# Kernel optimization log

Hardware: AMD Instinct MI355X
Metric: run time of the kernel (lower is better)

## Reference

```python
import jax, jax.numpy as jnp
import numpy as np

N = 65536          # query points (rays * samples per chunk)
C = 2048           # num_codes in code cloud
K = 16             # knn neighbors
CD = 64            # code_dim
IN_XYZ = 63        # positional-encoded xyz channels
IN_DIR = 27        # positional-encoded dir channels
W = 128            # decoder width (D=4, skips=[2])
DIST_SCALE = 2.0


def setup_inputs() -> dict:
    key = jax.random.key(0)
    ks = jax.random.split(key, 16)

    def glorot(k, shape):
        return jax.random.normal(k, shape, jnp.float32) / np.float32(np.sqrt(shape[0]))

    in_x = CD + IN_XYZ  # decoder in_channels_xyz = 127
    inp = {
        "indices": jnp.zeros((1,), jnp.int32),
        "query_points": jax.random.uniform(ks[0], (N, 3), jnp.float32),
        "xyzdir_embedded": jax.random.normal(ks[1], (N, IN_XYZ + IN_DIR), jnp.float32),
        "codes_position": jax.random.uniform(ks[2], (1, C, 3), jnp.float32),
        "codes": jax.random.normal(ks[3], (1, C, CD), jnp.float32) * 0.01,
        # decoder params
        "W0": glorot(ks[4], (in_x, W)), "b0": jnp.zeros((W,), jnp.float32),
        "W1": glorot(ks[5], (W, W)), "b1": jnp.zeros((W,), jnp.float32),
        "W2": glorot(ks[6], (W + in_x, W)), "b2": jnp.zeros((W,), jnp.float32),  # skip layer i=2
        "W3": glorot(ks[7], (W, W)), "b3": jnp.zeros((W,), jnp.float32),
        "Wf": glorot(ks[8], (W, W)), "bf": jnp.zeros((W,), jnp.float32),          # xyz_encoding_final
        "Wd": glorot(ks[9], (W + IN_DIR, W // 2)), "bd": jnp.zeros((W // 2,), jnp.float32),
        "Ws": glorot(ks[10], (W, 1)), "bs": jnp.zeros((1,), jnp.float32),
        "Wr": glorot(ks[11], (W // 2, 3)), "br": jnp.zeros((3,), jnp.float32),
    }
    return inp


def _knn_idx(q, c, k):
    # brute-force L2 knn (faiss replacement); indices only, no grad (torch no_grad)
    q = jax.lax.stop_gradient(q)
    c = jax.lax.stop_gradient(c)
    d2 = (jnp.sum(q * q, -1, keepdims=True)
          - 2.0 * q @ c.T
          + jnp.sum(c * c, -1))  # (N, C)
    _, idx = jax.lax.top_k(-d2, k)  # (N, K) nearest
    return idx


def reference(indices, query_points, xyzdir_embedded, codes_position, codes,
              W0, b0, W1, b1, W2, b2, W3, b3, Wf, bf, Wd, bd, Ws, bs, Wr, br):
    # --- CodeCloud.query ---
    cp = codes_position[indices][0]      # (C, 3)
    cc = codes[indices][0]               # (C, CD)
    idx = _knn_idx(query_points, cp, K)  # (N, K)
    neigh_pos = cp[idx]                  # (N, K, 3)
    sq = jnp.sum((query_points[:, None, :] - neigh_pos) ** 2, -1) + 1e-16  # (N, K)
    w = 1.0 / jnp.sqrt(sq) ** DIST_SCALE
    w = w / jnp.sum(w, -1, keepdims=True)
    neigh_codes = cc[idx]                # (N, K, CD)
    query_codes = jnp.einsum("nk,nkd->nd", w, neigh_codes)  # (N, CD)

    # --- IM_Decoder (D=4, W=128, skips=[2]) ---
    x = jnp.concatenate([query_codes, xyzdir_embedded], -1)  # (N, 127+27)
    in_x = CD + IN_XYZ
    input_xyz, input_dir = x[:, :in_x], x[:, in_x:]
    h = jax.nn.relu(input_xyz @ W0 + b0)
    h = jax.nn.relu(h @ W1 + b1)
    h = jax.nn.relu(jnp.concatenate([input_xyz, h], -1) @ W2 + b2)  # skip at i=2
    h = jax.nn.relu(h @ W3 + b3)
    sigma = h @ Ws + bs                       # (N, 1)
    final = h @ Wf + bf                       # (N, W)
    d = jax.nn.relu(jnp.concatenate([final, input_dir], -1) @ Wd + bd)
    rgb = d @ Wr + br                         # (N, 3)
    return jnp.concatenate([rgb, sigma], -1)  # (N, 4)
```

## Files before the change

kernel.cpp:

```cpp
#include <hip/hip_runtime.h>

#define N_Q   65536
#define N_C   2048
#define KNN_K 16
#define CDIM  64
#define SLCAP 128
#define KINF  0x7FFFFFFF
#define WSZ   108544

#define GN     16
#define GCELLS 4096
#define LCAP   448
#define LSTORE 512
#define NSLOT  8

typedef _Float16 half_t;
typedef float v4f __attribute__((ext_vector_type(4)));
typedef half_t v8h __attribute__((ext_vector_type(8)));
typedef unsigned short u16x8 __attribute__((ext_vector_type(8)));

#define ASTRIDE 136
#define DSTRIDE 40

__device__ __forceinline__ int dppx(int v, int j){
  if (j == 1) return __builtin_amdgcn_mov_dpp(v, 0xB1,  0xF, 0xF, true);
  if (j == 2) return __builtin_amdgcn_mov_dpp(v, 0x4E,  0xF, 0xF, true);
  if (j == 8) return __builtin_amdgcn_mov_dpp(v, 0x128, 0xF, 0xF, true);
  return __shfl_xor(v, j, 64);
}
__device__ __forceinline__ float dppxf(float v, int j){
  return __int_as_float(dppx(__float_as_int(v), j));
}

__device__ __forceinline__ int select16th(int x){
  int P = 0;
#pragma unroll
  for (int b = 30; b >= 0; --b){
    int cand = P | (1 << b);
    unsigned long long m = __ballot(x < cand);
    if ((int)__popcll(m) < 16) P = cand;
  }
  return P;
}

__device__ __forceinline__ int select16_tau(int x){
  int P = 0;
#pragma unroll
  for (int b = 30; b >= 11; --b){
    int cand = P | (1 << b);
    unsigned long long m = __ballot(x < cand);
    if ((int)__popcll(m) < 16) P = cand;
  }
  return P | 0x7FF;
}

__device__ __forceinline__ int knn_fallback(const float4* lp, float nqx,
                                            float nqy, float nqz, int lane){
  unsigned used = 0u;
  int keep = KINF;
#pragma unroll 1
  for (int rr = 0; rr < KNN_K; rr++){
    int best = KINF;
#pragma unroll 1
    for (int j = 0; j < 32; j++){
      int c = j*64 + lane;
      float4 P = lp[c];
      float s = fmaf(P.x, nqx, fmaf(P.y, nqy, fmaf(P.z, nqz, P.w)));
      int pv = (__float_as_int(s) & 0xFFFFF800) | c;
      pv = ((used >> j) & 1u) ? KINF : pv;
      best = min(best, pv);
    }
    int gm = best;
#pragma unroll
    for (int off2 = 1; off2 < 64; off2 <<= 1)
      gm = min(gm, __shfl_xor(gm, off2, 64));
    if (lane == rr) keep = gm;
    int gc = gm & 0x7FF;
    if ((gc & 63) == lane) used |= (1u << (gc >> 6));
  }
  return keep;
}

__global__ void wtrans_kernel(const float* W0, const float* W1, const float* W2,
                              const float* W3, const float* Wf, const float* Wd,
                              const int* indices, const float* cpos,
                              half_t* wt, float4* cpos4){
  int idx = blockIdx.x * 256 + threadIdx.x;
  if (idx >= 110592) return;
  if (idx >= WSZ){
    int i = idx - WSZ;
    const float* cp = cpos + (size_t)indices[0] * N_C * 3;
    float x = cp[i*3 + 0], y = cp[i*3 + 1], z = cp[i*3 + 2];
    cpos4[i] = make_float4(x, y, z, fmaf(x, x, fmaf(y, y, fmaf(z, z, 4.0f))));
    return;
  }
  int base, nt, mode;
  const float* src = W1;
  if (idx < 16384){ base = 0; nt = 8; mode = 1; }
  else if (idx < 32768){ base = 16384; nt = 8; mode = 0; src = W1; }
  else if (idx < 65536){ base = 32768; nt = 8; mode = 2; }
  else if (idx < 81920){ base = 65536; nt = 8; mode = 0; src = W3; }
  else if (idx < 98304){ base = 81920; nt = 8; mode = 0; src = Wf; }
  else { base = 98304; nt = 4; mode = 3; }
  int i = idx - base;
  int tile = i >> 9, e = i & 511;
  int lane = e >> 3, j = e & 7;
  int k0idx = tile / nt, tcol = tile - k0idx*nt;
  int n = tcol*16 + (lane & 15);
  int k = k0idx*32 + ((lane >> 4) << 3) + j;
  float val;
  if (mode == 0)      val = src[k*128 + n];
  else if (mode == 1) val = (k < 127) ? W0[k*128 + n] : 0.f;
  else if (mode == 2) val = (k == 127) ? 0.f
                           : ((k < 127) ? W2[k*128 + n] : W2[(k-1)*128 + n]);
  else                val = (k < 155) ? Wd[k*64 + n] : 0.f;
  wt[idx] = (half_t)val;
}

__global__ __launch_bounds__(512) void grid_kernel(const float4* cpos4,
    unsigned short* list, int* cnt){
  int lane = threadIdx.x & 63, wave = threadIdx.x >> 6;
  int c = blockIdx.x * 8 + wave;
  int cx = c & 15, cy = (c >> 4) & 15, cz = c >> 8;
  int lox = min(max(cx - 4, 0), 7);
  int loy = min(max(cy - 4, 0), 7);
  int loz = min(max(cz - 4, 0), 7);
  unsigned short* L = list + (size_t)c * LSTORE;
  int n = 0;
#pragma unroll 1
  for (int b = 0; b < 32; b++){
    int i = b * 64 + lane;
    float4 P = cpos4[i];
    int ix = min((int)(P.x * 16.0f), 15);
    int iy = min((int)(P.y * 16.0f), 15);
    int iz = min((int)(P.z * 16.0f), 15);
    bool in = ((unsigned)(ix - lox) < 9u) && ((unsigned)(iy - loy) < 9u) &&
              ((unsigned)(iz - loz) < 9u);
    unsigned long long m = __ballot(in);
    if (m){
      int mb = __builtin_amdgcn_mbcnt_hi((unsigned)(m >> 32),
               __builtin_amdgcn_mbcnt_lo((unsigned)m, 0));
      if (in && (n + mb) < LCAP) L[n + mb] = (unsigned short)i;
      n += (int)__popcll(m);
    }
  }
  if (lane == 0) cnt[c] = (n <= LCAP) ? n : 0;
}

__global__ __launch_bounds__(512, 6) void knn_kernel(const int* indices,
    const float* qpts, const float4* cpos4, const unsigned short* list,
    const int* cnt, const float* codes, const float* xyzdir,
    half_t* Ain, half_t* Din){
  __shared__ float4 lp[N_C];
  __shared__ int    sl[8*SLCAP];
  int tid = threadIdx.x;
  int lane = tid & 63, wave = tid >> 6;
  const float* cc = codes + (size_t)indices[0] * N_C * CDIM;

  for (int c = tid; c < N_C; c += 512) lp[c] = cpos4[c];
  __syncthreads();

  int q = blockIdx.x * 8 + wave;
  float qx = qpts[q*3 + 0];
  float qy = qpts[q*3 + 1];
  float qz = qpts[q*3 + 2];
  float nqx = -2.0f*qx, nqy = -2.0f*qy, nqz = -2.0f*qz;
  float qq = fmaf(qx, qx, fmaf(qy, qy, qz*qz));

  int cx = min((int)(qx * 16.0f), 15);
  int cy = min((int)(qy * 16.0f), 15);
  int cz = min((int)(qz * 16.0f), 15);
  int cell = cx | (cy << 4) | (cz << 8);
  int lox = min(max(cx - 4, 0), 7);
  int loy = min(max(cy - 4, 0), 7);
  int loz = min(max(cz - 4, 0), 7);
  int nl = cnt[cell];

  u16x8 cand8 = *(const u16x8*)(list + (size_t)cell * LSTORE + lane * 8);

  int p[NSLOT];
  int lanemin = KINF;
#pragma unroll
  for (int s = 0; s < NSLOT; s++){
    int j = lane*8 + s;
    int idx = (int)cand8[s] & 2047;
    float4 P = lp[idx];
    float sc = fmaf(P.x, nqx, fmaf(P.y, nqy, fmaf(P.z, nqz, P.w)));
    int pv = (__float_as_int(sc) & 0xFFFFF800) | idx;
    pv = (j < nl) ? pv : KINF;
    asm("" : "+v"(pv));
    p[s] = pv;
    lanemin = min(lanemin, pv);
  }

  int tau = select16_tau(lanemin);

  int* slw = &sl[wave * SLCAP];
  int n = 0;
#pragma unroll
  for (int s = 0; s < NSLOT; s++){
    bool c = (p[s] <= tau);
    unsigned long long m = __ballot(c);
    if (m){
      if (n <= 64){
        if (c){
          int mb = __builtin_amdgcn_mbcnt_hi((unsigned)(m >> 32),
                   __builtin_amdgcn_mbcnt_lo((unsigned)m, 0));
          slw[n + mb] = p[s];
        }
      }
      n += (int)__popcll(m);
    }
  }
  __builtin_amdgcn_wave_barrier();

  int keep = KINF;
  bool need_fb = true;
  if (n >= KNN_K && n <= 64){
    int x = (lane < n) ? slw[lane] : KINF;
    int P2 = select16th(x);
    unsigned long long wmask = __ballot(x <= P2);
    int pos = __builtin_amdgcn_mbcnt_hi((unsigned)(wmask >> 32),
              __builtin_amdgcn_mbcnt_lo((unsigned)wmask, 0));
    if (x <= P2) slw[pos] = x;
    __builtin_amdgcn_wave_barrier();
    keep = (lane < KNN_K) ? slw[lane] : KINF;

    float d2u = __int_as_float(P2 & 0xFFFFF800) - 4.0f + qq + 0.002f;
    float lofx = lox * 0.0625f, lofy = loy * 0.0625f, lofz = loz * 0.0625f;
    float cl = 1e9f;
    if (lox > 0) cl = fminf(cl, qx - lofx);
    if (lox < 7) cl = fminf(cl, lofx + 0.5625f - qx);
    if (loy > 0) cl = fminf(cl, qy - lofy);
    if (loy < 7) cl = fminf(cl, lofy + 0.5625f - qy);
    if (loz > 0) cl = fminf(cl, qz - lofz);
    if (loz < 7) cl = fminf(cl, lofz + 0.5625f - qz);
    need_fb = !(d2u <= cl * cl);
  }
  if (need_fb) keep = knn_fallback(lp, nqx, nqy, nqz, lane);

  int ci = keep & 0x7FF;
  float4 P = lp[ci];
  float dx = qx - P.x, dy = qy - P.y, dz = qz - P.z;
  float d2 = fmaf(dz, dz, fmaf(dy, dy, dx*dx));
  float w = 1.0f / (d2 + 1e-16f);
  float wm = (lane < KNN_K) ? w : 0.0f;
  wm += dppxf(wm, 1);
  wm += dppxf(wm, 2);
  wm += __shfl_xor(wm, 4, 64);
  wm += dppxf(wm, 8);
  float wn = w / wm;

  if (lane < KNN_K){
    slw[64 + 2*lane]     = ci;
    slw[64 + 2*lane + 1] = __float_as_int(wn);
  }
  __builtin_amdgcn_wave_barrier();

  float acc = 0.f;
#pragma unroll
  for (int i = 0; i < KNN_K; i++){
    int   cb = slw[64 + 2*i];
    float wb = __int_as_float(slw[64 + 2*i + 1]);
    acc = fmaf(wb, cc[cb*CDIM + lane], acc);
  }
  size_t arow = (size_t)q * ASTRIDE;
  Ain[arow + lane] = (half_t)acc;

  float xv = (lane < 63) ? xyzdir[(size_t)q*90 + lane] : 0.f;
  Ain[arow + 64 + lane] = (half_t)xv;
  if (lane < 8) Ain[arow + 128 + lane] = (half_t)0.f;
  if (lane < 40){
    float dv = (lane < 27) ? xyzdir[(size_t)q*90 + 63 + lane] : 0.f;
    Din[(size_t)q*DSTRIDE + lane] = (half_t)dv;
  }
}

template<int NCH, int NT>
__device__ inline void mfma_pl(const half_t* act, int astride, int rowbase,
                               const half_t* wlayer, int nt, int ktbase,
                               int tcolbase, v4f acc[2][NT], int lane){
  v8h breg[NCH*NT];
#pragma unroll
  for (int c = 0; c < NCH; c++){
#pragma unroll
    for (int t = 0; t < NT; t++){
      const half_t* bp = wlayer +
          ((size_t)(((ktbase + c)*nt + tcolbase + t) << 9) + (lane << 3));
      breg[c*NT + t] = *(const v8h*)bp;
    }
  }
  int m = lane & 15, quad = lane >> 4;
#pragma unroll
  for (int c = 0; c < NCH; c++){
    v8h a0 = *(const v8h*)&act[(rowbase + m)*astride + c*32 + quad*8];
    v8h a1 = *(const v8h*)&act[(rowbase + 16 + m)*astride + c*32 + quad*8];
#pragma unroll
    for (int t = 0; t < NT; t++){
      acc[0][t] = __builtin_amdgcn_mfma_f32_16x16x32_f16(a0, breg[c*NT + t], acc[0][t], 0, 0, 0);
      acc[1][t] = __builtin_amdgcn_mfma_f32_16x16x32_f16(a1, breg[c*NT + t], acc[1][t], 0, 0, 0);
    }
  }
}

template<int NT>
__device__ inline void epilogue64(v4f acc[2][NT], half_t* outb, int rowbase,
                                  int colbase, const float* bias, bool relu,
                                  int lane){
  int n = lane & 15, quad = lane >> 4;
#pragma unroll
  for (int t = 0; t < NT; t++){
    int col = colbase + t*16 + n;
    float bv = bias[col];
#pragma unroll
    for (int g = 0; g < 2; g++){
#pragma unroll
      for (int r = 0; r < 4; r++){
        float v = acc[g][t][r] + bv;
        if (relu) v = fmaxf(v, 0.f);
        outb[(rowbase + g*16 + quad*4 + r)*ASTRIDE + col] = (half_t)v;
      }
    }
  }
}

__global__ __launch_bounds__(512, 6) void mlp_mfma(
    const half_t* Ain, const half_t* Din, const half_t* wt,
    const float* b0, const float* b1, const float* b2, const float* b3,
    const float* bfb, const float* bdb,
    const float* Wsb, const float* bsb, const float* Wrb, const float* brb,
    float* out){
  __shared__ __align__(16) half_t Abuf[64*ASTRIDE];
  __shared__ __align__(16) half_t Pbuf[64*ASTRIDE];
  __shared__ __align__(16) half_t Qbuf[64*ASTRIDE];

  int tid = threadIdx.x, lane = tid & 63, wave = tid >> 6;
  int qbase = blockIdx.x * 64;

  for (int i = tid; i < 64*17; i += 512){
    int r = i / 17, c8 = i - r*17;
    *(uint4*)&Abuf[r*ASTRIDE + (c8 << 3)] =
        *(const uint4*)&Ain[(size_t)(qbase + r)*ASTRIDE + (c8 << 3)];
  }
  __syncthreads();

  int rowbase  = (wave >> 2) * 32;
  int colq     = wave & 3;
  int colbase  = colq * 32;
  int tcolbase = colq * 2;
  v4f acc[2][2];
  v4f accd[2][1];

  const half_t* wt0 = wt;
  const half_t* wt1 = wt + 16384;
  const half_t* wt2 = wt + 32768;
  const half_t* wt3 = wt + 65536;
  const half_t* wtf = wt + 81920;
  const half_t* wtd = wt + 98304;

#define ZACC22() { for (int g_ = 0; g_ < 2; g_++) for (int t_ = 0; t_ < 2; t_++) \
                   for (int e_ = 0; e_ < 4; e_++) acc[g_][t_][e_] = 0.f; }

  ZACC22();
  mfma_pl<4,2>(Abuf, ASTRIDE, rowbase, wt0, 8, 0, tcolbase, acc, lane);
  epilogue64<2>(acc, Pbuf, rowbase, colbase, b0, true, lane);
  __syncthreads();

  ZACC22();
  mfma_pl<4,2>(Pbuf, ASTRIDE, rowbase, wt1, 8, 0, tcolbase, acc, lane);
  epilogue64<2>(acc, Qbuf, rowbase, colbase, b1, true, lane);
  __syncthreads();

  ZACC22();
  mfma_pl<4,2>(Abuf, ASTRIDE, rowbase, wt2, 8, 0, tcolbase, acc, lane);
  mfma_pl<4,2>(Qbuf, ASTRIDE, rowbase, wt2, 8, 4, tcolbase, acc, lane);
  epilogue64<2>(acc, Pbuf, rowbase, colbase, b2, true, lane);
  __syncthreads();

  ZACC22();
  mfma_pl<4,2>(Pbuf, ASTRIDE, rowbase, wt3, 8, 0, tcolbase, acc, lane);
  epilogue64<2>(acc, Abuf, rowbase, colbase, b3, true, lane);
  __syncthreads();

  ZACC22();
  mfma_pl<4,2>(Abuf, ASTRIDE, rowbase, wtf, 8, 0, tcolbase, acc, lane);
  epilogue64<2>(acc, Pbuf, rowbase, colbase, bfb, false, lane);
  __syncthreads();

#pragma unroll
  for (int g_ = 0; g_ < 2; g_++)
#pragma unroll
    for (int e_ = 0; e_ < 4; e_++) accd[g_][0][e_] = 0.f;
  mfma_pl<4,1>(Pbuf, ASTRIDE, rowbase, wtd, 4, 0, colq, accd, lane);
  mfma_pl<1,1>(Din + (size_t)qbase*DSTRIDE, DSTRIDE, rowbase, wtd, 4, 4, colq,
               accd, lane);
  epilogue64<1>(accd, Qbuf, rowbase, colq * 16, bdb, true, lane);
  __syncthreads();

  {
    int q = tid >> 3, part = tid & 7;
    float s = 0.f;
#pragma unroll
    for (int k = 0; k < 16; k++){
      int kk = part*16 + k;
      s = fmaf((float)Abuf[q*ASTRIDE + kk], Wsb[kk], s);
    }
    s += __shfl_xor(s, 1, 64); s += __shfl_xor(s, 2, 64); s += __shfl_xor(s, 4, 64);

    float r3[3];
#pragma unroll
    for (int c2 = 0; c2 < 3; c2++){
      float rv = 0.f;
#pragma unroll
      for (int k = 0; k < 8; k++){
        int kk = part*8 + k;
        rv = fmaf((float)Qbuf[q*ASTRIDE + kk], Wrb[kk*3 + c2], rv);
      }
      rv += __shfl_xor(rv, 1, 64); rv += __shfl_xor(rv, 2, 64); rv += __shfl_xor(rv, 4, 64);
      r3[c2] = rv;
    }
    if (part == 0){
      size_t ob = ((size_t)(qbase + q)) * 4;
      out[ob + 0] = r3[0] + brb[0];
      out[ob + 1] = r3[1] + brb[1];
      out[ob + 2] = r3[2] + brb[2];
      out[ob + 3] = s + bsb[0];
    }
  }
}

extern "C" void kernel_launch(void* const* d_in, const int* in_sizes, int n_in,
                              void* d_out, int out_size, void* d_ws, size_t ws_size,
                              hipStream_t stream){
  (void)in_sizes; (void)n_in; (void)out_size; (void)ws_size;

  const int*   indices = (const int*)d_in[0];
  const float* qpts    = (const float*)d_in[1];
  const float* xyzdir  = (const float*)d_in[2];
  const float* cpos    = (const float*)d_in[3];
  const float* codes   = (const float*)d_in[4];
  const float* W0 = (const float*)d_in[5];
  const float* b0 = (const float*)d_in[6];
  const float* W1 = (const float*)d_in[7];
  const float* b1 = (const float*)d_in[8];
  const float* W2 = (const float*)d_in[9];
  const float* b2 = (const float*)d_in[10];
  const float* W3 = (const float*)d_in[11];
  const float* b3 = (const float*)d_in[12];
  const float* Wf = (const float*)d_in[13];
  const float* bf = (const float*)d_in[14];
  const float* Wd = (const float*)d_in[15];
  const float* bd = (const float*)d_in[16];
  const float* Ws = (const float*)d_in[17];
  const float* bs = (const float*)d_in[18];
  const float* Wr = (const float*)d_in[19];
  const float* br = (const float*)d_in[20];

  half_t* Ain            = (half_t*)d_ws;
  half_t* Din            = (half_t*)((char*)d_ws + 17825792);
  half_t* wt             = (half_t*)((char*)d_ws + 23068672);
  float4* cpos4          = (float4*)((char*)d_ws + 23285760);
  unsigned short* list   = (unsigned short*)((char*)d_ws + 23318528);
  int* cnt               = (int*)((char*)d_ws + 27512832);

  wtrans_kernel<<<(110592 + 255)/256, 256, 0, stream>>>(W0, W1, W2, W3, Wf, Wd,
                                                        indices, cpos, wt, cpos4);
  grid_kernel<<<GCELLS/8, 512, 0, stream>>>(cpos4, list, cnt);
  knn_kernel<<<N_Q/8, 512, 0, stream>>>(indices, qpts, cpos4, list, cnt,
                                        codes, xyzdir, Ain, Din);
  mlp_mfma<<<N_Q/64, 512, 0, stream>>>(Ain, Din, wt,
                                       b0, b1, b2, b3, bf, bd, Ws, bs, Wr, br,
                                       (float*)d_out);
}
```

Measured before the change: 201.6 us.

## Process two queries per wave in knn kernel with interleaved selection

Each wave now handles two query points at once, with the ballot-based radix selections, candidate compaction, weighting and code gathers interleaved for both queries. The grid halves and the shared staging area doubles. The goal is more instruction-level parallelism to hide the latency of the serial ballot chains and gathers, and to amortise the per-block load of code positions into LDS. The cost is higher register pressure under launch_bounds(512,6), fewer blocks, and fallback paths that may now serialize within a wave.

```diff
diff --git a/kernel.cpp b/kernel.cpp
--- a/kernel.cpp
+++ b/kernel.cpp
@@ -32,26 +32,35 @@
   return __int_as_float(dppx(__float_as_int(v), j));
 }
 
-__device__ __forceinline__ int select16th(int x){
-  int P = 0;
+__device__ __forceinline__ int mbcnt64(unsigned long long m){
+  return __builtin_amdgcn_mbcnt_hi((unsigned)(m >> 32),
+         __builtin_amdgcn_mbcnt_lo((unsigned)m, 0));
+}
+
+__device__ __forceinline__ void select16_tau2(int xA, int xB, int& tA, int& tB){
+  int PA = 0, PB = 0;
+#pragma unroll
+  for (int b = 30; b >= 11; --b){
+    unsigned long long mA = __ballot(xA < (PA | (1 << b)));
+    unsigned long long mB = __ballot(xB < (PB | (1 << b)));
+    if ((int)__popcll(mA) < 16) PA |= (1 << b);
+    if ((int)__popcll(mB) < 16) PB |= (1 << b);
+  }
+  tA = PA | 0x7FF;
+  tB = PB | 0x7FF;
+}
+
+__device__ __forceinline__ void select16th2(int xA, int xB, int& QA, int& QB){
+  int PA = 0, PB = 0;
 #pragma unroll
   for (int b = 30; b >= 0; --b){
-    int cand = P | (1 << b);
-    unsigned long long m = __ballot(x < cand);
-    if ((int)__popcll(m) < 16) P = cand;
-  }
-  return P;
-}
-
-__device__ __forceinline__ int select16_tau(int x){
-  int P = 0;
-#pragma unroll
-  for (int b = 30; b >= 11; --b){
-    int cand = P | (1 << b);
-    unsigned long long m = __ballot(x < cand);
-    if ((int)__popcll(m) < 16) P = cand;
-  }
-  return P | 0x7FF;
+    unsigned long long mA = __ballot(xA < (PA | (1 << b)));
+    unsigned long long mB = __ballot(xB < (PB | (1 << b)));
+    if ((int)__popcll(mA) < 16) PA |= (1 << b);
+    if ((int)__popcll(mB) < 16) PB |= (1 << b);
+  }
+  QA = PA;
+  QB = PB;
 }
 
 __device__ __forceinline__ int knn_fallback(const float4* lp, float nqx,
@@ -138,8 +147,7 @@
               ((unsigned)(iz - loz) < 9u);
     unsigned long long m = __ballot(in);
     if (m){
-      int mb = __builtin_amdgcn_mbcnt_hi((unsigned)(m >> 32),
-               __builtin_amdgcn_mbcnt_lo((unsigned)m, 0));
+      int mb = mbcnt64(m);
       if (in && (n + mb) < LCAP) L[n + mb] = (unsigned short)i;
       n += (int)__popcll(m);
     }
@@ -152,7 +160,7 @@
     const int* cnt, const float* codes, const float* xyzdir,
     half_t* Ain, half_t* Din){
   __shared__ float4 lp[N_C];
-  __shared__ int    sl[8*SLCAP];
+  __shared__ int    sl[16*SLCAP];
   int tid = threadIdx.x;
   int lane = tid & 63, wave = tid >> 6;
   const float* cc = codes + (size_t)indices[0] * N_C * CDIM;
@@ -160,119 +168,176 @@
   for (int c = tid; c < N_C; c += 512) lp[c] = cpos4[c];
   __syncthreads();
 
-  int q = blockIdx.x * 8 + wave;
-  float qx = qpts[q*3 + 0];
-  float qy = qpts[q*3 + 1];
-  float qz = qpts[q*3 + 2];
-  float nqx = -2.0f*qx, nqy = -2.0f*qy, nqz = -2.0f*qz;
-  float qq = fmaf(qx, qx, fmaf(qy, qy, qz*qz));
-
-  int cx = min((int)(qx * 16.0f), 15);
-  int cy = min((int)(qy * 16.0f), 15);
-  int cz = min((int)(qz * 16.0f), 15);
-  int cell = cx | (cy << 4) | (cz << 8);
-  int lox = min(max(cx - 4, 0), 7);
-  int loy = min(max(cy - 4, 0), 7);
-  int loz = min(max(cz - 4, 0), 7);
-  int nl = cnt[cell];
-
-  u16x8 cand8 = *(const u16x8*)(list + (size_t)cell * LSTORE + lane * 8);
-
-  int p[NSLOT];
-  int lanemin = KINF;
+  int qA = blockIdx.x * 16 + wave * 2;
+  int qB = qA + 1;
+  float qxA = qpts[qA*3 + 0], qyA = qpts[qA*3 + 1], qzA = qpts[qA*3 + 2];
+  float qxB = qpts[qB*3 + 0], qyB = qpts[qB*3 + 1], qzB = qpts[qB*3 + 2];
+  float nqxA = -2.0f*qxA, nqyA = -2.0f*qyA, nqzA = -2.0f*qzA;
+  float nqxB = -2.0f*qxB, nqyB = -2.0f*qyB, nqzB = -2.0f*qzB;
+  float qqA = fmaf(qxA, qxA, fmaf(qyA, qyA, qzA*qzA));
+  float qqB = fmaf(qxB, qxB, fmaf(qyB, qyB, qzB*qzB));
+
+  int cxA = min((int)(qxA * 16.0f), 15);
+  int cyA = min((int)(qyA * 16.0f), 15);
+  int czA = min((int)(qzA * 16.0f), 15);
+  int cxB = min((int)(qxB * 16.0f), 15);
+  int cyB = min((int)(qyB * 16.0f), 15);
+  int czB = min((int)(qzB * 16.0f), 15);
+  int cellA = cxA | (cyA << 4) | (czA << 8);
+  int cellB = cxB | (cyB << 4) | (czB << 8);
+  int loxA = min(max(cxA - 4, 0), 7), loyA = min(max(cyA - 4, 0), 7),
+      lozA = min(max(czA - 4, 0), 7);
+  int loxB = min(max(cxB - 4, 0), 7), loyB = min(max(cyB - 4, 0), 7),
+      lozB = min(max(czB - 4, 0), 7);
+  int nlA = cnt[cellA];
+  int nlB = cnt[cellB];
+
+  u16x8 c8A = *(const u16x8*)(list + (size_t)cellA * LSTORE + lane * 8);
+  u16x8 c8B = *(const u16x8*)(list + (size_t)cellB * LSTORE + lane * 8);
+
+  int pA[NSLOT], pB[NSLOT];
+  int lmA = KINF, lmB = KINF;
 #pragma unroll
   for (int s = 0; s < NSLOT; s++){
     int j = lane*8 + s;
-    int idx = (int)cand8[s] & 2047;
-    float4 P = lp[idx];
-    float sc = fmaf(P.x, nqx, fmaf(P.y, nqy, fmaf(P.z, nqz, P.w)));
-    int pv = (__float_as_int(sc) & 0xFFFFF800) | idx;
-    pv = (j < nl) ? pv : KINF;
-    asm("" : "+v"(pv));
-    p[s] = pv;
-    lanemin = min(lanemin, pv);
-  }
-
-  int tau = select16_tau(lanemin);
-
-  int* slw = &sl[wave * SLCAP];
-  int n = 0;
+    int iA = (int)c8A[s] & 2047;
+    int iB = (int)c8B[s] & 2047;
+    float4 PA = lp[iA];
+    float4 PB = lp[iB];
+    float sA = fmaf(PA.x, nqxA, fmaf(PA.y, nqyA, fmaf(PA.z, nqzA, PA.w)));
+    float sB = fmaf(PB.x, nqxB, fmaf(PB.y, nqyB, fmaf(PB.z, nqzB, PB.w)));
+    int pvA = (__float_as_int(sA) & 0xFFFFF800) | iA;
+    int pvB = (__float_as_int(sB) & 0xFFFFF800) | iB;
+    pvA = (j < nlA) ? pvA : KINF;
+    pvB = (j < nlB) ? pvB : KINF;
+    asm("" : "+v"(pvA));
+    asm("" : "+v"(pvB));
+    pA[s] = pvA; pB[s] = pvB;
+    lmA = min(lmA, pvA);
+    lmB = min(lmB, pvB);
+  }
+
+  int tauA, tauB;
+  select16_tau2(lmA, lmB, tauA, tauB);
+
+  int* slwA = &sl[(wave*2 + 0) * SLCAP];
+  int* slwB = &sl[(wave*2 + 1) * SLCAP];
+  int nA = 0, nB = 0;
 #pragma unroll
   for (int s = 0; s < NSLOT; s++){
-    bool c = (p[s] <= tau);
-    unsigned long long m = __ballot(c);
-    if (m){
-      if (n <= 64){
-        if (c){
-          int mb = __builtin_amdgcn_mbcnt_hi((unsigned)(m >> 32),
-                   __builtin_amdgcn_mbcnt_lo((unsigned)m, 0));
-          slw[n + mb] = p[s];
-        }
-      }
-      n += (int)__popcll(m);
-    }
+    bool cA = (pA[s] <= tauA);
+    bool cB = (pB[s] <= tauB);
+    unsigned long long mA = __ballot(cA);
+    unsigned long long mB = __ballot(cB);
+    int mbA = mbcnt64(mA);
+    int mbB = mbcnt64(mB);
+    if (cA && nA <= 64) slwA[nA + mbA] = pA[s];
+    if (cB && nB <= 64) slwB[nB + mbB] = pB[s];
+    nA += (int)__popcll(mA);
+    nB += (int)__popcll(mB);
   }
   __builtin_amdgcn_wave_barrier();
 
-  int keep = KINF;
-  bool need_fb = true;
-  if (n >= KNN_K && n <= 64){
-    int x = (lane < n) ? slw[lane] : KINF;
-    int P2 = select16th(x);
-    unsigned long long wmask = __ballot(x <= P2);
-    int pos = __builtin_amdgcn_mbcnt_hi((unsigned)(wmask >> 32),
-              __builtin_amdgcn_mbcnt_lo((unsigned)wmask, 0));
-    if (x <= P2) slw[pos] = x;
-    __builtin_amdgcn_wave_barrier();
-    keep = (lane < KNN_K) ? slw[lane] : KINF;
-
-    float d2u = __int_as_float(P2 & 0xFFFFF800) - 4.0f + qq + 0.002f;
-    float lofx = lox * 0.0625f, lofy = loy * 0.0625f, lofz = loz * 0.0625f;
+  bool okA = (nA >= KNN_K && nA <= 64);
+  bool okB = (nB >= KNN_K && nB <= 64);
+  int xA = (lane < nA) ? slwA[lane] : KINF;
+  int xB = (lane < nB) ? slwB[lane] : KINF;
+  int P2A, P2B;
+  select16th2(xA, xB, P2A, P2B);
+  unsigned long long wmkA = __ballot(xA <= P2A);
+  unsigned long long wmkB = __ballot(xB <= P2B);
+  int posA = mbcnt64(wmkA);
+  int posB = mbcnt64(wmkB);
+  if (xA <= P2A) slwA[posA] = xA;
+  if (xB <= P2B) slwB[posB] = xB;
+  __builtin_amdgcn_wave_barrier();
+
+  int keepA = KINF, keepB = KINF;
+  bool fbA = true, fbB = true;
+  if (okA){
+    keepA = (lane < KNN_K) ? slwA[lane] : KINF;
+    float d2u = __int_as_float(P2A & 0xFFFFF800) - 4.0f + qqA + 0.002f;
+    float lofx = loxA * 0.0625f, lofy = loyA * 0.0625f, lofz = lozA * 0.0625f;
     float cl = 1e9f;
-    if (lox > 0) cl = fminf(cl, qx - lofx);
-    if (lox < 7) cl = fminf(cl, lofx + 0.5625f - qx);
-    if (loy > 0) cl = fminf(cl, qy - lofy);
-    if (loy < 7) cl = fminf(cl, lofy + 0.5625f - qy);
-    if (loz > 0) cl = fminf(cl, qz - lofz);
-    if (loz < 7) cl = fminf(cl, lofz + 0.5625f - qz);
-    need_fb = !(d2u <= cl * cl);
-  }
-  if (need_fb) keep = knn_fallback(lp, nqx, nqy, nqz, lane);
-
-  int ci = keep & 0x7FF;
-  float4 P = lp[ci];
-  float dx = qx - P.x, dy = qy - P.y, dz = qz - P.z;
-  float d2 = fmaf(dz, dz, fmaf(dy, dy, dx*dx));
-  float w = 1.0f / (d2 + 1e-16f);
-  float wm = (lane < KNN_K) ? w : 0.0f;
-  wm += dppxf(wm, 1);
-  wm += dppxf(wm, 2);
-  wm += __shfl_xor(wm, 4, 64);
-  wm += dppxf(wm, 8);
-  float wn = w / wm;
+    if (loxA > 0) cl = fminf(cl, qxA - lofx);
+    if (loxA < 7) cl = fminf(cl, lofx + 0.5625f - qxA);
+    if (loyA > 0) cl = fminf(cl, qyA - lofy);
+    if (loyA < 7) cl = fminf(cl, lofy + 0.5625f - qyA);
+    if (lozA > 0) cl = fminf(cl, qzA - lofz);
+    if (lozA < 7) cl = fminf(cl, lofz + 0.5625f - qzA);
+    fbA = !(d2u <= cl * cl);
+  }
+  if (okB){
+    keepB = (lane < KNN_K) ? slwB[lane] : KINF;
+    float d2u = __int_as_float(P2B & 0xFFFFF800) - 4.0f + qqB + 0.002f;
+    float lofx = loxB * 0.0625f, lofy = loyB * 0.0625f, lofz = lozB * 0.0625f;
+    float cl = 1e9f;
+    if (loxB > 0) cl = fminf(cl, qxB - lofx);
+    if (loxB < 7) cl = fminf(cl, lofx + 0.5625f - qxB);
+    if (loyB > 0) cl = fminf(cl, qyB - lofy);
+    if (loyB < 7) cl = fminf(cl, lofy + 0.5625f - qyB);
+    if (lozB > 0) cl = fminf(cl, qzB - lofz);
+    if (lozB < 7) cl = fminf(cl, lofz + 0.5625f - qzB);
+    fbB = !(d2u <= cl * cl);
+  }
+  if (fbA) keepA = knn_fallback(lp, nqxA, nqyA, nqzA, lane);
+  if (fbB) keepB = knn_fallback(lp, nqxB, nqyB, nqzB, lane);
+
+  int ciA = keepA & 0x7FF;
+  int ciB = keepB & 0x7FF;
+  float4 PA4 = lp[ciA];
+  float4 PB4 = lp[ciB];
+  float dxA = qxA - PA4.x, dyA = qyA - PA4.y, dzA = qzA - PA4.z;
+  float dxB = qxB - PB4.x, dyB = qyB - PB4.y, dzB = qzB - PB4.z;
+  float d2A = fmaf(dzA, dzA, fmaf(dyA, dyA, dxA*dxA));
+  float d2B = fmaf(dzB, dzB, fmaf(dyB, dyB, dxB*dxB));
+  float wA = 1.0f / (d2A + 1e-16f);
+  float wB = 1.0f / (d2B + 1e-16f);
+  float wmA = (lane < KNN_K) ? wA : 0.0f;
+  float wmB = (lane < KNN_K) ? wB : 0.0f;
+  wmA += dppxf(wmA, 1);            wmB += dppxf(wmB, 1);
+  wmA += dppxf(wmA, 2);            wmB += dppxf(wmB, 2);
+  wmA += __shfl_xor(wmA, 4, 64);   wmB += __shfl_xor(wmB, 4, 64);
+  wmA += dppxf(wmA, 8);            wmB += dppxf(wmB, 8);
+  float wnA = wA / wmA;
+  float wnB = wB / wmB;
 
   if (lane < KNN_K){
-    slw[64 + 2*lane]     = ci;
-    slw[64 + 2*lane + 1] = __float_as_int(wn);
+    slwA[64 + 2*lane]     = ciA;
+    slwA[64 + 2*lane + 1] = __float_as_int(wnA);
+    slwB[64 + 2*lane]     = ciB;
+    slwB[64 + 2*lane + 1] = __float_as_int(wnB);
   }
   __builtin_amdgcn_wave_barrier();
 
-  float acc = 0.f;
+  float accA = 0.f, accB = 0.f;
 #pragma unroll
   for (int i = 0; i < KNN_K; i++){
-    int   cb = slw[64 + 2*i];
-    float wb = __int_as_float(slw[64 + 2*i + 1]);
-    acc = fmaf(wb, cc[cb*CDIM + lane], acc);
-  }
-  size_t arow = (size_t)q * ASTRIDE;
-  Ain[arow + lane] = (half_t)acc;
-
-  float xv = (lane < 63) ? xyzdir[(size_t)q*90 + lane] : 0.f;
-  Ain[arow + 64 + lane] = (half_t)xv;
-  if (lane < 8) Ain[arow + 128 + lane] = (half_t)0.f;
+    int   cbA = slwA[64 + 2*i];
+    int   cbB = slwB[64 + 2*i];
+    float wbA = __int_as_float(slwA[64 + 2*i + 1]);
+    float wbB = __int_as_float(slwB[64 + 2*i + 1]);
+    accA = fmaf(wbA, cc[cbA*CDIM + lane], accA);
+    accB = fmaf(wbB, cc[cbB*CDIM + lane], accB);
+  }
+  size_t arowA = (size_t)qA * ASTRIDE;
+  size_t arowB = (size_t)qB * ASTRIDE;
+  Ain[arowA + lane] = (half_t)accA;
+  Ain[arowB + lane] = (half_t)accB;
+
+  float xvA = (lane < 63) ? xyzdir[(size_t)qA*90 + lane] : 0.f;
+  float xvB = (lane < 63) ? xyzdir[(size_t)qB*90 + lane] : 0.f;
+  Ain[arowA + 64 + lane] = (half_t)xvA;
+  Ain[arowB + 64 + lane] = (half_t)xvB;
+  if (lane < 8){
+    Ain[arowA + 128 + lane] = (half_t)0.f;
+    Ain[arowB + 128 + lane] = (half_t)0.f;
+  }
   if (lane < 40){
-    float dv = (lane < 27) ? xyzdir[(size_t)q*90 + 63 + lane] : 0.f;
-    Din[(size_t)q*DSTRIDE + lane] = (half_t)dv;
+    float dvA = (lane < 27) ? xyzdir[(size_t)qA*90 + 63 + lane] : 0.f;
+    float dvB = (lane < 27) ? xyzdir[(size_t)qB*90 + 63 + lane] : 0.f;
+    Din[(size_t)qA*DSTRIDE + lane] = (half_t)dvA;
+    Din[(size_t)qB*DSTRIDE + lane] = (half_t)dvB;
   }
 }
 
@@ -466,8 +531,8 @@
   wtrans_kernel<<<(110592 + 255)/256, 256, 0, stream>>>(W0, W1, W2, W3, Wf, Wd,
                                                         indices, cpos, wt, cpos4);
   grid_kernel<<<GCELLS/8, 512, 0, stream>>>(cpos4, list, cnt);
-  knn_kernel<<<N_Q/8, 512, 0, stream>>>(indices, qpts, cpos4, list, cnt,
-                                        codes, xyzdir, Ain, Din);
+  knn_kernel<<<N_Q/16, 512, 0, stream>>>(indices, qpts, cpos4, list, cnt,
+                                         codes, xyzdir, Ain, Din);
   mlp_mfma<<<N_Q/64, 512, 0, stream>>>(Ain, Din, wt,
                                        b0, b1, b2, b3, bf, bd, Ws, bs, Wr, br,
                                        (float*)d_out);
```

Result: no change. 199.7 us (-0.9%).
